# Kernel tuning notes

Measured on AMD Instinct MI355X. Metric: run time of the kernel, lower is better.

Reference implementation:

```python
import jax, jax.numpy as jnp
import numpy as np

EPS = 1e-8

def cos_sim(a, b, axis=-1):
    # torch.nn.functional.cosine_similarity: dot / max(|a|*|b|, eps)
    num = jnp.sum(a * b, axis=axis)
    den = jnp.maximum(jnp.linalg.norm(a, axis=axis) * jnp.linalg.norm(b, axis=axis), EPS)
    return num / den

def address_similarity(address, addresses):
    # address: [b, d], addresses: [b, n, d] -> [b, n]
    return cos_sim(address[:, None, :], addresses, axis=2)

def kv_insert(state_k, state_v, k, x, eps=EPS):
    # state_k/state_v: [b, n, d]; k: [b, d]; x: [b, d] (or [1, d], broadcast)
    alpha = cos_sim(k[:, None, :], state_k, axis=2)          # [b, n]
    alpha = jnp.where(alpha > eps, alpha, 0.0)
    return (1.0 - alpha)[..., None] * state_v + alpha[..., None] * x[:, None, :]

def replace(new_value, prev_value, tensr):
    # new_value/prev_value: [b, d]; tensr: [b, n, d]
    sim_to = cos_sim(prev_value[:, None, :], tensr, axis=2)  # [b, n]
    return tensr * (1.0 - sim_to)[..., None] + sim_to[..., None] * new_value[:, None, :]

def select_address(address, addresses, list_of_values):
    cs = address_similarity(address, addresses)              # [b, n]
    return [jnp.sum(values * cs[..., None], axis=1) for values in list_of_values]

def setup_inputs() -> dict:
    key = jax.random.key(0)
    ks = jax.random.split(key, 5)
    B, N, D = 32, 2048, 128
    return {
        "at_addr": jax.random.normal(ks[0], (B, D), dtype=jnp.float32),
        "addresses": jax.random.normal(ks[1], (B, N, D), dtype=jnp.float32),
        "tags": jax.random.normal(ks[2], (B, N, D), dtype=jnp.float32),
        "col1": jax.random.normal(ks[3], (B, N, D), dtype=jnp.float32),
        "col2": jax.random.normal(ks[4], (B, N, D), dtype=jnp.float32),
        "zero_vec": jnp.zeros((D,), dtype=jnp.float32),
        "gc_steps": 2,
    }

def reference(at_addr, addresses, tags, col1, col2, zero_vec, gc_steps):
    B = at_addr.shape[0]
    zv = jnp.broadcast_to(zero_vec[None, :], (B, zero_vec.shape[0]))
    # dereference the App node
    fn_addr, arg_addr = select_address(at_addr, addresses, [col1, col2])
    fn_tag, param_addr, body_addr = select_address(fn_addr, addresses, [tags, col1, col2])
    a_tag, a_l, a_r = select_address(arg_addr, addresses, [tags, col1, col2])
    # substitute arg into param's slot (globally scoped vars)
    tags = kv_insert(addresses, tags, param_addr, a_tag)
    col1 = kv_insert(addresses, col1, param_addr, a_l)
    col2 = kv_insert(addresses, col2, param_addr, a_r)
    col1 = replace(arg_addr, param_addr, col1)
    col2 = replace(arg_addr, param_addr, col2)
    # write the fn body over the App node
    b_tag, b_l, b_r = select_address(body_addr, addresses, [tags, col1, col2])
    tags = kv_insert(addresses, tags, at_addr, b_tag)
    col1 = kv_insert(addresses, col1, at_addr, b_l)
    col2 = kv_insert(addresses, col2, at_addr, b_r)
    # garbage collection
    for _ in range(gc_steps):
        for gaddr in (fn_addr, param_addr, body_addr):
            tags = kv_insert(addresses, tags, gaddr, zv)
            col1 = kv_insert(addresses, col1, gaddr, zv)
            col2 = kv_insert(addresses, col2, gaddr, zv)
    return (tags, col1, col2)
```

## Files before the change

### kernel.cpp

```cpp
#include <hip/hip_runtime.h>

#define EPSF 1e-8f
#define DD 128

__device__ __forceinline__ float4 ld4(const float* p){ return *reinterpret_cast<const float4*>(p); }
__device__ __forceinline__ void st4(float* p, const float4& v){ *reinterpret_cast<float4*>(p) = v; }
__device__ __forceinline__ float dot4(const float4& a, const float4& b){
  return a.x*b.x + a.y*b.y + a.z*b.z + a.w*b.w;
}
__device__ __forceinline__ void fma4(float4& acc, const float4& a, float s){
  acc.x += a.x*s; acc.y += a.y*s; acc.z += a.z*s; acc.w += a.w*s;
}
__device__ __forceinline__ float4 mix4(float a, const float4& v, const float4& x){
  float4 r;
  r.x = (1.f-a)*v.x + a*x.x;
  r.y = (1.f-a)*v.y + a*x.y;
  r.z = (1.f-a)*v.z + a*x.z;
  r.w = (1.f-a)*v.w + a*x.w;
  return r;
}
__device__ __forceinline__ float red16(float v){
  v += __shfl_xor(v, 1);
  v += __shfl_xor(v, 2);
  v += __shfl_xor(v, 4);
  v += __shfl_xor(v, 8);
  return v;
}
__device__ __forceinline__ void block_red16(float* red, int g, int l, int t,
                                            const float4& accA, const float4& accB,
                                            float* dst){
  red[g*DD + l*4+0] = accA.x;
  red[g*DD + l*4+1] = accA.y;
  red[g*DD + l*4+2] = accA.z;
  red[g*DD + l*4+3] = accA.w;
  red[g*DD + 64 + l*4+0] = accB.x;
  red[g*DD + 64 + l*4+1] = accB.y;
  red[g*DD + 64 + l*4+2] = accB.z;
  red[g*DD + 64 + l*4+3] = accB.w;
  __syncthreads();
  if (t < DD){
    float s = 0.f;
    #pragma unroll
    for (int q = 0; q < 16; ++q) s += red[q*DD + t];
    dst[t] = s;
  }
  __syncthreads();
}

__global__ __launch_bounds__(256) void kA(const float* __restrict__ at,
                                          const float* __restrict__ addr,
                                          const float* __restrict__ col1,
                                          const float* __restrict__ col2,
                                          float* __restrict__ cs0,
                                          float* __restrict__ naf,
                                          float* __restrict__ part,
                                          int B, int N, int chunks){
  __shared__ float red[16*DD];
  int blk = blockIdx.x;
  int b = blk / chunks, c = blk % chunks;
  int rows = N / chunks, n0 = c * rows;
  int t = threadIdx.x, g = t >> 4, l = t & 15;
  size_t bN = (size_t)b * N;

  const float* atp = at + (size_t)b*DD;
  float4 atA = ld4(atp + l*4), atB = ld4(atp + 64 + l*4);
  float nat = sqrtf(red16(dot4(atA, atA) + dot4(atB, atB)));

  float4 accFA = make_float4(0,0,0,0), accFB = accFA, accAA = accFA, accAB = accFA;
  #pragma unroll 2
  for (int r = g; r < rows; r += 16){
    size_t n = (size_t)n0 + r;
    size_t base = (bN + n)*DD;
    float4 aA  = ld4(addr + base + l*4), aB  = ld4(addr + base + 64 + l*4);
    float4 c1A = ld4(col1 + base + l*4), c1B = ld4(col1 + base + 64 + l*4);
    float4 c2A = ld4(col2 + base + l*4), c2B = ld4(col2 + base + 64 + l*4);
    float dp = red16(dot4(atA, aA) + dot4(atB, aB));
    float n2 = red16(dot4(aA, aA) + dot4(aB, aB));
    float na = sqrtf(n2);
    float cs = dp / fmaxf(nat * na, EPSF);
    if (l == 0){ cs0[bN + n] = cs; naf[bN + n] = na; }
    fma4(accFA, c1A, cs); fma4(accFB, c1B, cs);
    fma4(accAA, c2A, cs); fma4(accAB, c2B, cs);
  }
  block_red16(red, g, l, t, accFA, accFB, part + (((size_t)(0*B + b))*chunks + c)*DD);
  block_red16(red, g, l, t, accAA, accAB, part + (((size_t)(1*B + b))*chunks + c)*DD);
}

__global__ void kFin(const float* __restrict__ part, float* __restrict__ dst,
                     int nvec, int B, int chunks){
  int i = blockIdx.x*blockDim.x + threadIdx.x;
  int total = nvec * B * DD;
  if (i >= total) return;
  int d = i & (DD-1);
  int vb = i >> 7;
  const float* p = part + ((size_t)vb*chunks)*DD + d;
  float s = 0.f;
  for (int c = 0; c < chunks; ++c) s += p[(size_t)c*DD];
  dst[i] = s;
}

__global__ __launch_bounds__(256) void kB(const float* __restrict__ addr,
                                          const float* __restrict__ tags,
                                          const float* __restrict__ col1,
                                          const float* __restrict__ col2,
                                          const float* __restrict__ vecs,
                                          const float* __restrict__ naf,
                                          float* __restrict__ csfn,
                                          float* __restrict__ part,
                                          int B, int N, int chunks){
  __shared__ float red[16*DD];
  int blk = blockIdx.x;
  int b = blk / chunks, c = blk % chunks;
  int rows = N / chunks, n0 = c * rows;
  int t = threadIdx.x, g = t >> 4, l = t & 15;
  size_t bN = (size_t)b * N;

  const float* fnp = vecs + ((size_t)0*B + b)*DD;
  const float* agp = vecs + ((size_t)1*B + b)*DD;
  float4 fnA = ld4(fnp + l*4), fnB = ld4(fnp + 64 + l*4);
  float4 agA = ld4(agp + l*4), agB = ld4(agp + 64 + l*4);
  float nfn = sqrtf(red16(dot4(fnA, fnA) + dot4(fnB, fnB)));
  float nag = sqrtf(red16(dot4(agA, agA) + dot4(agB, agB)));

  float4 z = make_float4(0,0,0,0);
  float4 accPA=z, accPB=z, accBA=z, accBB=z, accTA=z, accTB=z, accLA=z, accLB=z, accRA=z, accRB=z;
  #pragma unroll 2
  for (int r = g; r < rows; r += 16){
    size_t n = (size_t)n0 + r;
    size_t base = (bN + n)*DD;
    float4 aA  = ld4(addr + base + l*4), aB  = ld4(addr + base + 64 + l*4);
    float4 t4A = ld4(tags + base + l*4), t4B = ld4(tags + base + 64 + l*4);
    float4 c1A = ld4(col1 + base + l*4), c1B = ld4(col1 + base + 64 + l*4);
    float4 c2A = ld4(col2 + base + l*4), c2B = ld4(col2 + base + 64 + l*4);
    float na = naf[bN + n];
    float dfn = red16(dot4(fnA, aA) + dot4(fnB, aB));
    float dag = red16(dot4(agA, aA) + dot4(agB, aB));
    float cf = dfn / fmaxf(nfn*na, EPSF);
    float ca = dag / fmaxf(nag*na, EPSF);
    if (l == 0) csfn[bN + n] = cf;
    fma4(accPA, c1A, cf); fma4(accPB, c1B, cf);
    fma4(accBA, c2A, cf); fma4(accBB, c2B, cf);
    fma4(accTA, t4A, ca); fma4(accTB, t4B, ca);
    fma4(accLA, c1A, ca); fma4(accLB, c1B, ca);
    fma4(accRA, c2A, ca); fma4(accRB, c2B, ca);
  }
  block_red16(red, g, l, t, accPA, accPB, part + (((size_t)(0*B + b))*chunks + c)*DD);
  block_red16(red, g, l, t, accBA, accBB, part + (((size_t)(1*B + b))*chunks + c)*DD);
  block_red16(red, g, l, t, accTA, accTB, part + (((size_t)(2*B + b))*chunks + c)*DD);
  block_red16(red, g, l, t, accLA, accLB, part + (((size_t)(3*B + b))*chunks + c)*DD);
  block_red16(red, g, l, t, accRA, accRB, part + (((size_t)(4*B + b))*chunks + c)*DD);
}

__global__ __launch_bounds__(256) void kC(const float* __restrict__ addr,
                                          const float* __restrict__ tags,
                                          const float* __restrict__ col1,
                                          const float* __restrict__ col2,
                                          const float* __restrict__ vecs,
                                          const float* __restrict__ naf,
                                          float* __restrict__ alphap,
                                          float* __restrict__ csbody,
                                          float* __restrict__ s1f,
                                          float* __restrict__ s2f,
                                          float* __restrict__ part,
                                          int B, int N, int chunks){
  __shared__ float red[16*DD];
  int blk = blockIdx.x;
  int b = blk / chunks, c = blk % chunks;
  int rows = N / chunks, n0 = c * rows;
  int t = threadIdx.x, g = t >> 4, l = t & 15;
  size_t bN = (size_t)b * N;

  size_t BD = (size_t)B*DD;
  const float* vp = vecs + (size_t)b*DD;
  float4 agA = ld4(vp + 1*BD + l*4), agB = ld4(vp + 1*BD + 64 + l*4);
  float4 pmA = ld4(vp + 2*BD + l*4), pmB = ld4(vp + 2*BD + 64 + l*4);
  float4 bdA = ld4(vp + 3*BD + l*4), bdB = ld4(vp + 3*BD + 64 + l*4);
  float4 xtA = ld4(vp + 4*BD + l*4), xtB = ld4(vp + 4*BD + 64 + l*4);
  float4 xlA = ld4(vp + 5*BD + l*4), xlB = ld4(vp + 5*BD + 64 + l*4);
  float4 xrA = ld4(vp + 6*BD + l*4), xrB = ld4(vp + 6*BD + 64 + l*4);
  float npm = sqrtf(red16(dot4(pmA, pmA) + dot4(pmB, pmB)));
  float nbd = sqrtf(red16(dot4(bdA, bdA) + dot4(bdB, bdB)));

  float4 z = make_float4(0,0,0,0);
  float4 accTA=z, accTB=z, accLA=z, accLB=z, accRA=z, accRB=z;
  #pragma unroll 2
  for (int r = g; r < rows; r += 16){
    size_t n = (size_t)n0 + r;
    size_t base = (bN + n)*DD;
    float4 aA  = ld4(addr + base + l*4), aB  = ld4(addr + base + 64 + l*4);
    float4 t4A = ld4(tags + base + l*4), t4B = ld4(tags + base + 64 + l*4);
    float4 c1A = ld4(col1 + base + l*4), c1B = ld4(col1 + base + 64 + l*4);
    float4 c2A = ld4(col2 + base + l*4), c2B = ld4(col2 + base + 64 + l*4);
    float na = naf[bN + n];
    float dp = red16(dot4(pmA, aA) + dot4(pmB, aB));
    float db = red16(dot4(bdA, aA) + dot4(bdB, aB));
    float csp = dp / fmaxf(npm*na, EPSF);
    float ap  = csp > EPSF ? csp : 0.f;
    float csb = db / fmaxf(nbd*na, EPSF);

    float4 tnA  = mix4(ap, t4A, xtA), tnB  = mix4(ap, t4B, xtB);
    float4 c1nA = mix4(ap, c1A, xlA), c1nB = mix4(ap, c1B, xlB);
    float4 c2nA = mix4(ap, c2A, xrA), c2nB = mix4(ap, c2B, xrB);
    float d1  = red16(dot4(pmA, c1nA) + dot4(pmB, c1nB));
    float n21 = red16(dot4(c1nA, c1nA) + dot4(c1nB, c1nB));
    float s1 = d1 / fmaxf(npm * sqrtf(n21), EPSF);
    float4 c1fA = mix4(s1, c1nA, agA), c1fB = mix4(s1, c1nB, agB);
    float d2  = red16(dot4(pmA, c2nA) + dot4(pmB, c2nB));
    float n22 = red16(dot4(c2nA, c2nA) + dot4(c2nB, c2nB));
    float s2 = d2 / fmaxf(npm * sqrtf(n22), EPSF);
    float4 c2fA = mix4(s2, c2nA, agA), c2fB = mix4(s2, c2nB, agB);

    if (l == 0){
      alphap[bN + n] = ap;
      csbody[bN + n] = csb;
      s1f[bN + n] = s1;
      s2f[bN + n] = s2;
    }
    fma4(accTA, tnA,  csb); fma4(accTB, tnB,  csb);
    fma4(accLA, c1fA, csb); fma4(accLB, c1fB, csb);
    fma4(accRA, c2fA, csb); fma4(accRB, c2fB, csb);
  }
  block_red16(red, g, l, t, accTA, accTB, part + (((size_t)(0*B + b))*chunks + c)*DD);
  block_red16(red, g, l, t, accLA, accLB, part + (((size_t)(1*B + b))*chunks + c)*DD);
  block_red16(red, g, l, t, accRA, accRB, part + (((size_t)(2*B + b))*chunks + c)*DD);
}

__global__ __launch_bounds__(256) void kE(const float* __restrict__ tags,
                                          const float* __restrict__ col1,
                                          const float* __restrict__ col2,
                                          float* __restrict__ o_t,
                                          float* __restrict__ o_1,
                                          float* __restrict__ o_2,
                                          const float* __restrict__ cs0,
                                          const float* __restrict__ csfn,
                                          const float* __restrict__ alphap,
                                          const float* __restrict__ csbody,
                                          const float* __restrict__ s1f,
                                          const float* __restrict__ s2f,
                                          const float* __restrict__ vecs,
                                          const float* __restrict__ zv,
                                          const int* __restrict__ gcp,
                                          int B, int N){
  size_t i = (size_t)blockIdx.x*blockDim.x + threadIdx.x;
  size_t total = (size_t)B*N*(DD/4);
  if (i >= total) return;
  int l = (int)(i & 31);
  size_t bn = i >> 5;
  int b = (int)(bn / (size_t)N);

  float ap = alphap[bn], s1 = s1f[bn], s2 = s2f[bn];
  float c0 = cs0[bn], cf = csfn[bn], cb = csbody[bn];
  float aat = c0 > EPSF ? c0 : 0.f;
  float af  = cf > EPSF ? cf : 0.f;
  float ab  = cb > EPSF ? cb : 0.f;
  float q = (1.f-af)*(1.f-ap)*(1.f-ab);
  int gc = gcp[0];
  float P = 1.f;
  for (int k = 0; k < gc; ++k) P *= q;

  size_t BD = (size_t)B*DD;
  const float* vb = vecs + (size_t)b*DD + (size_t)l*4;
  float4 ag = ld4(vb + 1*BD);
  float4 xt = ld4(vb + 4*BD), xl = ld4(vb + 5*BD), xr = ld4(vb + 6*BD);
  float4 bt = ld4(vb + 7*BD), bl = ld4(vb + 8*BD), br = ld4(vb + 9*BD);
  float4 z4 = ld4(zv + l*4);

  size_t off = bn*DD + (size_t)l*4;
  float4 t4 = ld4(tags + off), c1 = ld4(col1 + off), c2 = ld4(col2 + off);

  float4 tn  = mix4(ap, t4, xt);
  float4 c1f = mix4(s1, mix4(ap, c1, xl), ag);
  float4 c2f = mix4(s2, mix4(ap, c2, xr), ag);

  float4 u;
  u = mix4(aat, tn, bt);
  u.x = P*u.x + (1.f-P)*z4.x; u.y = P*u.y + (1.f-P)*z4.y;
  u.z = P*u.z + (1.f-P)*z4.z; u.w = P*u.w + (1.f-P)*z4.w;
  st4(o_t + off, u);
  u = mix4(aat, c1f, bl);
  u.x = P*u.x + (1.f-P)*z4.x; u.y = P*u.y + (1.f-P)*z4.y;
  u.z = P*u.z + (1.f-P)*z4.z; u.w = P*u.w + (1.f-P)*z4.w;
  st4(o_1 + off, u);
  u = mix4(aat, c2f, br);
  u.x = P*u.x + (1.f-P)*z4.x; u.y = P*u.y + (1.f-P)*z4.y;
  u.z = P*u.z + (1.f-P)*z4.z; u.w = P*u.w + (1.f-P)*z4.w;
  st4(o_2 + off, u);
}

extern "C" void kernel_launch(void* const* d_in, const int* in_sizes, int n_in,
                              void* d_out, int out_size, void* d_ws, size_t ws_size,
                              hipStream_t stream){
  const float* at   = (const float*)d_in[0];
  const float* addr = (const float*)d_in[1];
  const float* tags = (const float*)d_in[2];
  const float* col1 = (const float*)d_in[3];
  const float* col2 = (const float*)d_in[4];
  const float* zv   = (const float*)d_in[5];
  const int*   gc   = (const int*)d_in[6];

  int Dd = in_sizes[5];
  int B  = in_sizes[0] / Dd;
  int N  = in_sizes[1] / in_sizes[0];
  (void)Dd;

  size_t S  = (size_t)B * N;
  size_t BD = (size_t)B * DD;

  int CH = 32;
  while (CH > 1){
    size_t need = (7*S + 10*BD + (size_t)5*B*CH*DD) * sizeof(float);
    if (need <= ws_size && (N % CH) == 0) break;
    CH >>= 1;
  }

  float* w = (float*)d_ws;
  float* cs0    = w;
  float* csfn   = w + S;
  float* alphap = w + 2*S;
  float* csbody = w + 3*S;
  float* s1f    = w + 4*S;
  float* s2f    = w + 5*S;
  float* naf    = w + 6*S;
  float* vecs   = w + 7*S;
  float* part   = vecs + 10*BD;

  float* o_t = (float*)d_out;
  float* o_1 = o_t + (size_t)B*N*DD;
  float* o_2 = o_1 + (size_t)B*N*DD;

  dim3 blk(256);
  dim3 grid(B*CH);

  kA<<<grid, blk, 0, stream>>>(at, addr, col1, col2, cs0, naf, part, B, N, CH);
  {
    int tot = 2*B*DD;
    kFin<<<(tot+255)/256, 256, 0, stream>>>(part, vecs + 0*BD, 2, B, CH);
  }
  kB<<<grid, blk, 0, stream>>>(addr, tags, col1, col2, vecs, naf, csfn, part, B, N, CH);
  {
    int tot = 5*B*DD;
    kFin<<<(tot+255)/256, 256, 0, stream>>>(part, vecs + 2*BD, 5, B, CH);
  }
  kC<<<grid, blk, 0, stream>>>(addr, tags, col1, col2, vecs, naf, alphap, csbody,
                               s1f, s2f, part, B, N, CH);
  {
    int tot = 3*B*DD;
    kFin<<<(tot+255)/256, 256, 0, stream>>>(part, vecs + 7*BD, 3, B, CH);
  }
  {
    size_t tot = (size_t)B*N*(DD/4);
    kE<<<(unsigned)((tot+255)/256), 256, 0, stream>>>(tags, col1, col2, o_t, o_1, o_2,
                                                      cs0, csfn, alphap, csbody,
                                                      s1f, s2f, vecs, zv, gc, B, N);
  }
}
```

Before: 126.3 us.

## Fuse all phases into one cooperative persistent kernel with grid syncs

Replaces the separate similarity, partial-reduce and final-update kernels with one cooperative kernel. The phases are separated by grid.sync(), so launch gaps between the seven stages go away. The final update is remapped so each block writes the same row chunk it processed earlier, which may improve cache reuse. In exchange it adds six grid-wide barriers and caps the grid size by occupancy, with a register limit from launch_bounds(256,4); a per-phase multi-launch fallback remains if the cooperative launch fails.

Measured after the change: 450.0 us. +256.5%, slower.

```diff
diff --git a/kernel.cpp b/kernel.cpp
--- a/kernel.cpp
+++ b/kernel.cpp
@@ -1,4 +1,7 @@
 #include <hip/hip_runtime.h>
+#include <hip/hip_cooperative_groups.h>
+
+namespace cg = cooperative_groups;
 
 #define EPSF 1e-8f
 #define DD 128
@@ -47,244 +50,230 @@
   __syncthreads();
 }
 
-__global__ __launch_bounds__(256) void kA(const float* __restrict__ at,
-                                          const float* __restrict__ addr,
-                                          const float* __restrict__ col1,
-                                          const float* __restrict__ col2,
-                                          float* __restrict__ cs0,
-                                          float* __restrict__ naf,
-                                          float* __restrict__ part,
-                                          int B, int N, int chunks){
+__global__ __launch_bounds__(256, 4) void kFused(
+    const float* __restrict__ at,   const float* __restrict__ addr,
+    const float* __restrict__ tags, const float* __restrict__ col1,
+    const float* __restrict__ col2, const float* __restrict__ zv,
+    const int* __restrict__ gcp,
+    float* __restrict__ o_t, float* __restrict__ o_1, float* __restrict__ o_2,
+    float* __restrict__ w, int B, int N, int CH, int onlyPhase)
+{
+  cg::grid_group grid = cg::this_grid();
   __shared__ float red[16*DD];
-  int blk = blockIdx.x;
-  int b = blk / chunks, c = blk % chunks;
-  int rows = N / chunks, n0 = c * rows;
-  int t = threadIdx.x, g = t >> 4, l = t & 15;
-  size_t bN = (size_t)b * N;
-
-  const float* atp = at + (size_t)b*DD;
-  float4 atA = ld4(atp + l*4), atB = ld4(atp + 64 + l*4);
-  float nat = sqrtf(red16(dot4(atA, atA) + dot4(atB, atB)));
-
-  float4 accFA = make_float4(0,0,0,0), accFB = accFA, accAA = accFA, accAB = accFA;
-  #pragma unroll 2
-  for (int r = g; r < rows; r += 16){
-    size_t n = (size_t)n0 + r;
-    size_t base = (bN + n)*DD;
-    float4 aA  = ld4(addr + base + l*4), aB  = ld4(addr + base + 64 + l*4);
-    float4 c1A = ld4(col1 + base + l*4), c1B = ld4(col1 + base + 64 + l*4);
-    float4 c2A = ld4(col2 + base + l*4), c2B = ld4(col2 + base + 64 + l*4);
-    float dp = red16(dot4(atA, aA) + dot4(atB, aB));
-    float n2 = red16(dot4(aA, aA) + dot4(aB, aB));
-    float na = sqrtf(n2);
-    float cs = dp / fmaxf(nat * na, EPSF);
-    if (l == 0){ cs0[bN + n] = cs; naf[bN + n] = na; }
-    fma4(accFA, c1A, cs); fma4(accFB, c1B, cs);
-    fma4(accAA, c2A, cs); fma4(accAB, c2B, cs);
-  }
-  block_red16(red, g, l, t, accFA, accFB, part + (((size_t)(0*B + b))*chunks + c)*DD);
-  block_red16(red, g, l, t, accAA, accAB, part + (((size_t)(1*B + b))*chunks + c)*DD);
-}
-
-__global__ void kFin(const float* __restrict__ part, float* __restrict__ dst,
-                     int nvec, int B, int chunks){
-  int i = blockIdx.x*blockDim.x + threadIdx.x;
-  int total = nvec * B * DD;
-  if (i >= total) return;
-  int d = i & (DD-1);
-  int vb = i >> 7;
-  const float* p = part + ((size_t)vb*chunks)*DD + d;
-  float s = 0.f;
-  for (int c = 0; c < chunks; ++c) s += p[(size_t)c*DD];
-  dst[i] = s;
-}
-
-__global__ __launch_bounds__(256) void kB(const float* __restrict__ addr,
-                                          const float* __restrict__ tags,
-                                          const float* __restrict__ col1,
-                                          const float* __restrict__ col2,
-                                          const float* __restrict__ vecs,
-                                          const float* __restrict__ naf,
-                                          float* __restrict__ csfn,
-                                          float* __restrict__ part,
-                                          int B, int N, int chunks){
-  __shared__ float red[16*DD];
-  int blk = blockIdx.x;
-  int b = blk / chunks, c = blk % chunks;
-  int rows = N / chunks, n0 = c * rows;
-  int t = threadIdx.x, g = t >> 4, l = t & 15;
-  size_t bN = (size_t)b * N;
-
-  const float* fnp = vecs + ((size_t)0*B + b)*DD;
-  const float* agp = vecs + ((size_t)1*B + b)*DD;
-  float4 fnA = ld4(fnp + l*4), fnB = ld4(fnp + 64 + l*4);
-  float4 agA = ld4(agp + l*4), agB = ld4(agp + 64 + l*4);
-  float nfn = sqrtf(red16(dot4(fnA, fnA) + dot4(fnB, fnB)));
-  float nag = sqrtf(red16(dot4(agA, agA) + dot4(agB, agB)));
-
-  float4 z = make_float4(0,0,0,0);
-  float4 accPA=z, accPB=z, accBA=z, accBB=z, accTA=z, accTB=z, accLA=z, accLB=z, accRA=z, accRB=z;
-  #pragma unroll 2
-  for (int r = g; r < rows; r += 16){
-    size_t n = (size_t)n0 + r;
-    size_t base = (bN + n)*DD;
-    float4 aA  = ld4(addr + base + l*4), aB  = ld4(addr + base + 64 + l*4);
-    float4 t4A = ld4(tags + base + l*4), t4B = ld4(tags + base + 64 + l*4);
-    float4 c1A = ld4(col1 + base + l*4), c1B = ld4(col1 + base + 64 + l*4);
-    float4 c2A = ld4(col2 + base + l*4), c2B = ld4(col2 + base + 64 + l*4);
-    float na = naf[bN + n];
-    float dfn = red16(dot4(fnA, aA) + dot4(fnB, aB));
-    float dag = red16(dot4(agA, aA) + dot4(agB, aB));
-    float cf = dfn / fmaxf(nfn*na, EPSF);
-    float ca = dag / fmaxf(nag*na, EPSF);
-    if (l == 0) csfn[bN + n] = cf;
-    fma4(accPA, c1A, cf); fma4(accPB, c1B, cf);
-    fma4(accBA, c2A, cf); fma4(accBB, c2B, cf);
-    fma4(accTA, t4A, ca); fma4(accTB, t4B, ca);
-    fma4(accLA, c1A, ca); fma4(accLB, c1B, ca);
-    fma4(accRA, c2A, ca); fma4(accRB, c2B, ca);
-  }
-  block_red16(red, g, l, t, accPA, accPB, part + (((size_t)(0*B + b))*chunks + c)*DD);
-  block_red16(red, g, l, t, accBA, accBB, part + (((size_t)(1*B + b))*chunks + c)*DD);
-  block_red16(red, g, l, t, accTA, accTB, part + (((size_t)(2*B + b))*chunks + c)*DD);
-  block_red16(red, g, l, t, accLA, accLB, part + (((size_t)(3*B + b))*chunks + c)*DD);
-  block_red16(red, g, l, t, accRA, accRB, part + (((size_t)(4*B + b))*chunks + c)*DD);
-}
-
-__global__ __launch_bounds__(256) void kC(const float* __restrict__ addr,
-                                          const float* __restrict__ tags,
-                                          const float* __restrict__ col1,
-                                          const float* __restrict__ col2,
-                                          const float* __restrict__ vecs,
-                                          const float* __restrict__ naf,
-                                          float* __restrict__ alphap,
-                                          float* __restrict__ csbody,
-                                          float* __restrict__ s1f,
-                                          float* __restrict__ s2f,
-                                          float* __restrict__ part,
-                                          int B, int N, int chunks){
-  __shared__ float red[16*DD];
-  int blk = blockIdx.x;
-  int b = blk / chunks, c = blk % chunks;
-  int rows = N / chunks, n0 = c * rows;
-  int t = threadIdx.x, g = t >> 4, l = t & 15;
-  size_t bN = (size_t)b * N;
-
-  size_t BD = (size_t)B*DD;
-  const float* vp = vecs + (size_t)b*DD;
-  float4 agA = ld4(vp + 1*BD + l*4), agB = ld4(vp + 1*BD + 64 + l*4);
-  float4 pmA = ld4(vp + 2*BD + l*4), pmB = ld4(vp + 2*BD + 64 + l*4);
-  float4 bdA = ld4(vp + 3*BD + l*4), bdB = ld4(vp + 3*BD + 64 + l*4);
-  float4 xtA = ld4(vp + 4*BD + l*4), xtB = ld4(vp + 4*BD + 64 + l*4);
-  float4 xlA = ld4(vp + 5*BD + l*4), xlB = ld4(vp + 5*BD + 64 + l*4);
-  float4 xrA = ld4(vp + 6*BD + l*4), xrB = ld4(vp + 6*BD + 64 + l*4);
-  float npm = sqrtf(red16(dot4(pmA, pmA) + dot4(pmB, pmB)));
-  float nbd = sqrtf(red16(dot4(bdA, bdA) + dot4(bdB, bdB)));
-
-  float4 z = make_float4(0,0,0,0);
-  float4 accTA=z, accTB=z, accLA=z, accLB=z, accRA=z, accRB=z;
-  #pragma unroll 2
-  for (int r = g; r < rows; r += 16){
-    size_t n = (size_t)n0 + r;
-    size_t base = (bN + n)*DD;
-    float4 aA  = ld4(addr + base + l*4), aB  = ld4(addr + base + 64 + l*4);
-    float4 t4A = ld4(tags + base + l*4), t4B = ld4(tags + base + 64 + l*4);
-    float4 c1A = ld4(col1 + base + l*4), c1B = ld4(col1 + base + 64 + l*4);
-    float4 c2A = ld4(col2 + base + l*4), c2B = ld4(col2 + base + 64 + l*4);
-    float na = naf[bN + n];
-    float dp = red16(dot4(pmA, aA) + dot4(pmB, aB));
-    float db = red16(dot4(bdA, aA) + dot4(bdB, aB));
-    float csp = dp / fmaxf(npm*na, EPSF);
-    float ap  = csp > EPSF ? csp : 0.f;
-    float csb = db / fmaxf(nbd*na, EPSF);
-
-    float4 tnA  = mix4(ap, t4A, xtA), tnB  = mix4(ap, t4B, xtB);
-    float4 c1nA = mix4(ap, c1A, xlA), c1nB = mix4(ap, c1B, xlB);
-    float4 c2nA = mix4(ap, c2A, xrA), c2nB = mix4(ap, c2B, xrB);
-    float d1  = red16(dot4(pmA, c1nA) + dot4(pmB, c1nB));
-    float n21 = red16(dot4(c1nA, c1nA) + dot4(c1nB, c1nB));
-    float s1 = d1 / fmaxf(npm * sqrtf(n21), EPSF);
-    float4 c1fA = mix4(s1, c1nA, agA), c1fB = mix4(s1, c1nB, agB);
-    float d2  = red16(dot4(pmA, c2nA) + dot4(pmB, c2nB));
-    float n22 = red16(dot4(c2nA, c2nA) + dot4(c2nB, c2nB));
-    float s2 = d2 / fmaxf(npm * sqrtf(n22), EPSF);
-    float4 c2fA = mix4(s2, c2nA, agA), c2fB = mix4(s2, c2nB, agB);
-
-    if (l == 0){
-      alphap[bN + n] = ap;
-      csbody[bN + n] = csb;
-      s1f[bN + n] = s1;
-      s2f[bN + n] = s2;
-    }
-    fma4(accTA, tnA,  csb); fma4(accTB, tnB,  csb);
-    fma4(accLA, c1fA, csb); fma4(accLB, c1fB, csb);
-    fma4(accRA, c2fA, csb); fma4(accRB, c2fB, csb);
-  }
-  block_red16(red, g, l, t, accTA, accTB, part + (((size_t)(0*B + b))*chunks + c)*DD);
-  block_red16(red, g, l, t, accLA, accLB, part + (((size_t)(1*B + b))*chunks + c)*DD);
-  block_red16(red, g, l, t, accRA, accRB, part + (((size_t)(2*B + b))*chunks + c)*DD);
-}
-
-__global__ __launch_bounds__(256) void kE(const float* __restrict__ tags,
-                                          const float* __restrict__ col1,
-                                          const float* __restrict__ col2,
-                                          float* __restrict__ o_t,
-                                          float* __restrict__ o_1,
-                                          float* __restrict__ o_2,
-                                          const float* __restrict__ cs0,
-                                          const float* __restrict__ csfn,
-                                          const float* __restrict__ alphap,
-                                          const float* __restrict__ csbody,
-                                          const float* __restrict__ s1f,
-                                          const float* __restrict__ s2f,
-                                          const float* __restrict__ vecs,
-                                          const float* __restrict__ zv,
-                                          const int* __restrict__ gcp,
-                                          int B, int N){
-  size_t i = (size_t)blockIdx.x*blockDim.x + threadIdx.x;
-  size_t total = (size_t)B*N*(DD/4);
-  if (i >= total) return;
-  int l = (int)(i & 31);
-  size_t bn = i >> 5;
-  int b = (int)(bn / (size_t)N);
-
-  float ap = alphap[bn], s1 = s1f[bn], s2 = s2f[bn];
-  float c0 = cs0[bn], cf = csfn[bn], cb = csbody[bn];
-  float aat = c0 > EPSF ? c0 : 0.f;
-  float af  = cf > EPSF ? cf : 0.f;
-  float ab  = cb > EPSF ? cb : 0.f;
-  float q = (1.f-af)*(1.f-ap)*(1.f-ab);
-  int gc = gcp[0];
-  float P = 1.f;
-  for (int k = 0; k < gc; ++k) P *= q;
-
-  size_t BD = (size_t)B*DD;
-  const float* vb = vecs + (size_t)b*DD + (size_t)l*4;
-  float4 ag = ld4(vb + 1*BD);
-  float4 xt = ld4(vb + 4*BD), xl = ld4(vb + 5*BD), xr = ld4(vb + 6*BD);
-  float4 bt = ld4(vb + 7*BD), bl = ld4(vb + 8*BD), br = ld4(vb + 9*BD);
-  float4 z4 = ld4(zv + l*4);
-
-  size_t off = bn*DD + (size_t)l*4;
-  float4 t4 = ld4(tags + off), c1 = ld4(col1 + off), c2 = ld4(col2 + off);
-
-  float4 tn  = mix4(ap, t4, xt);
-  float4 c1f = mix4(s1, mix4(ap, c1, xl), ag);
-  float4 c2f = mix4(s2, mix4(ap, c2, xr), ag);
-
-  float4 u;
-  u = mix4(aat, tn, bt);
-  u.x = P*u.x + (1.f-P)*z4.x; u.y = P*u.y + (1.f-P)*z4.y;
-  u.z = P*u.z + (1.f-P)*z4.z; u.w = P*u.w + (1.f-P)*z4.w;
-  st4(o_t + off, u);
-  u = mix4(aat, c1f, bl);
-  u.x = P*u.x + (1.f-P)*z4.x; u.y = P*u.y + (1.f-P)*z4.y;
-  u.z = P*u.z + (1.f-P)*z4.z; u.w = P*u.w + (1.f-P)*z4.w;
-  st4(o_1 + off, u);
-  u = mix4(aat, c2f, br);
-  u.x = P*u.x + (1.f-P)*z4.x; u.y = P*u.y + (1.f-P)*z4.y;
-  u.z = P*u.z + (1.f-P)*z4.z; u.w = P*u.w + (1.f-P)*z4.w;
-  st4(o_2 + off, u);
+
+  const size_t S  = (size_t)B * N;
+  const size_t BD = (size_t)B * DD;
+  float* cs0    = w;
+  float* csfn   = w + S;
+  float* alphap = w + 2*S;
+  float* csbody = w + 3*S;
+  float* s1f    = w + 4*S;
+  float* s2f    = w + 5*S;
+  float* naf    = w + 6*S;
+  float* vecs   = w + 7*S;
+  float* part   = vecs + 10*BD;
+
+  const int blk = blockIdx.x;
+  const int b = blk / CH, c = blk % CH;
+  const int rows = N / CH, n0 = c * rows;
+  const int t = threadIdx.x, g = t >> 4, l = t & 15;
+  const size_t bN = (size_t)b * N;
+  const int G = gridDim.x;
+
+  if (onlyPhase < 0 || onlyPhase == 0){
+    const float* atp = at + (size_t)b*DD;
+    float4 atA = ld4(atp + l*4), atB = ld4(atp + 64 + l*4);
+    float nat = sqrtf(red16(dot4(atA, atA) + dot4(atB, atB)));
+    float4 accFA = make_float4(0,0,0,0), accFB = accFA, accAA = accFA, accAB = accFA;
+    #pragma unroll 2
+    for (int r = g; r < rows; r += 16){
+      size_t n = (size_t)n0 + r;
+      size_t base = (bN + n)*DD;
+      float4 aA  = ld4(addr + base + l*4), aB  = ld4(addr + base + 64 + l*4);
+      float4 c1A = ld4(col1 + base + l*4), c1B = ld4(col1 + base + 64 + l*4);
+      float4 c2A = ld4(col2 + base + l*4), c2B = ld4(col2 + base + 64 + l*4);
+      float dp = red16(dot4(atA, aA) + dot4(atB, aB));
+      float n2 = red16(dot4(aA, aA) + dot4(aB, aB));
+      float na = sqrtf(n2);
+      float cs = dp / fmaxf(nat * na, EPSF);
+      if (l == 0){ cs0[bN + n] = cs; naf[bN + n] = na; }
+      fma4(accFA, c1A, cs); fma4(accFB, c1B, cs);
+      fma4(accAA, c2A, cs); fma4(accAB, c2B, cs);
+    }
+    block_red16(red, g, l, t, accFA, accFB, part + ((size_t)(0*B + b)*CH + c)*DD);
+    block_red16(red, g, l, t, accAA, accAB, part + ((size_t)(1*B + b)*CH + c)*DD);
+  }
+  if (onlyPhase < 0) grid.sync();
+
+  if (onlyPhase < 0 || onlyPhase == 1){
+    int tot = 2*B*DD;
+    for (int i = blk*256 + t; i < tot; i += G*256){
+      int vb = i >> 7, d = i & (DD-1);
+      const float* p = part + ((size_t)vb*CH)*DD + d;
+      float s = 0.f;
+      for (int cc = 0; cc < CH; ++cc) s += p[(size_t)cc*DD];
+      vecs[i] = s;
+    }
+  }
+  if (onlyPhase < 0) grid.sync();
+
+  if (onlyPhase < 0 || onlyPhase == 2){
+    const float* fnp = vecs + (size_t)b*DD;
+    const float* agp = vecs + BD + (size_t)b*DD;
+    float4 fnA = ld4(fnp + l*4), fnB = ld4(fnp + 64 + l*4);
+    float4 agA = ld4(agp + l*4), agB = ld4(agp + 64 + l*4);
+    float nfn = sqrtf(red16(dot4(fnA, fnA) + dot4(fnB, fnB)));
+    float nag = sqrtf(red16(dot4(agA, agA) + dot4(agB, agB)));
+    float4 z = make_float4(0,0,0,0);
+    float4 accPA=z, accPB=z, accBA=z, accBB=z, accTA=z, accTB=z, accLA=z, accLB=z, accRA=z, accRB=z;
+    #pragma unroll 2
+    for (int r = g; r < rows; r += 16){
+      size_t n = (size_t)n0 + r;
+      size_t base = (bN + n)*DD;
+      float4 aA  = ld4(addr + base + l*4), aB  = ld4(addr + base + 64 + l*4);
+      float4 t4A = ld4(tags + base + l*4), t4B = ld4(tags + base + 64 + l*4);
+      float4 c1A = ld4(col1 + base + l*4), c1B = ld4(col1 + base + 64 + l*4);
+      float4 c2A = ld4(col2 + base + l*4), c2B = ld4(col2 + base + 64 + l*4);
+      float na = naf[bN + n];
+      float dfn = red16(dot4(fnA, aA) + dot4(fnB, aB));
+      float dag = red16(dot4(agA, aA) + dot4(agB, aB));
+      float cf = dfn / fmaxf(nfn*na, EPSF);
+      float ca = dag / fmaxf(nag*na, EPSF);
+      if (l == 0) csfn[bN + n] = cf;
+      fma4(accPA, c1A, cf); fma4(accPB, c1B, cf);
+      fma4(accBA, c2A, cf); fma4(accBB, c2B, cf);
+      fma4(accTA, t4A, ca); fma4(accTB, t4B, ca);
+      fma4(accLA, c1A, ca); fma4(accLB, c1B, ca);
+      fma4(accRA, c2A, ca); fma4(accRB, c2B, ca);
+    }
+    block_red16(red, g, l, t, accPA, accPB, part + ((size_t)(0*B + b)*CH + c)*DD);
+    block_red16(red, g, l, t, accBA, accBB, part + ((size_t)(1*B + b)*CH + c)*DD);
+    block_red16(red, g, l, t, accTA, accTB, part + ((size_t)(2*B + b)*CH + c)*DD);
+    block_red16(red, g, l, t, accLA, accLB, part + ((size_t)(3*B + b)*CH + c)*DD);
+    block_red16(red, g, l, t, accRA, accRB, part + ((size_t)(4*B + b)*CH + c)*DD);
+  }
+  if (onlyPhase < 0) grid.sync();
+
+  if (onlyPhase < 0 || onlyPhase == 3){
+    int tot = 5*B*DD;
+    for (int i = blk*256 + t; i < tot; i += G*256){
+      int vb = i >> 7, d = i & (DD-1);
+      const float* p = part + ((size_t)vb*CH)*DD + d;
+      float s = 0.f;
+      for (int cc = 0; cc < CH; ++cc) s += p[(size_t)cc*DD];
+      vecs[2*BD + i] = s;
+    }
+  }
+  if (onlyPhase < 0) grid.sync();
+
+  if (onlyPhase < 0 || onlyPhase == 4){
+    const float* vp = vecs + (size_t)b*DD;
+    float4 agA = ld4(vp + 1*BD + l*4), agB = ld4(vp + 1*BD + 64 + l*4);
+    float4 pmA = ld4(vp + 2*BD + l*4), pmB = ld4(vp + 2*BD + 64 + l*4);
+    float4 bdA = ld4(vp + 3*BD + l*4), bdB = ld4(vp + 3*BD + 64 + l*4);
+    float4 xtA = ld4(vp + 4*BD + l*4), xtB = ld4(vp + 4*BD + 64 + l*4);
+    float4 xlA = ld4(vp + 5*BD + l*4), xlB = ld4(vp + 5*BD + 64 + l*4);
+    float4 xrA = ld4(vp + 6*BD + l*4), xrB = ld4(vp + 6*BD + 64 + l*4);
+    float npm = sqrtf(red16(dot4(pmA, pmA) + dot4(pmB, pmB)));
+    float nbd = sqrtf(red16(dot4(bdA, bdA) + dot4(bdB, bdB)));
+    float4 z = make_float4(0,0,0,0);
+    float4 accTA=z, accTB=z, accLA=z, accLB=z, accRA=z, accRB=z;
+    #pragma unroll 2
+    for (int r = g; r < rows; r += 16){
+      size_t n = (size_t)n0 + r;
+      size_t base = (bN + n)*DD;
+      float4 aA  = ld4(addr + base + l*4), aB  = ld4(addr + base + 64 + l*4);
+      float4 t4A = ld4(tags + base + l*4), t4B = ld4(tags + base + 64 + l*4);
+      float4 c1A = ld4(col1 + base + l*4), c1B = ld4(col1 + base + 64 + l*4);
+      float4 c2A = ld4(col2 + base + l*4), c2B = ld4(col2 + base + 64 + l*4);
+      float na = naf[bN + n];
+      float dp = red16(dot4(pmA, aA) + dot4(pmB, aB));
+      float db = red16(dot4(bdA, aA) + dot4(bdB, aB));
+      float csp = dp / fmaxf(npm*na, EPSF);
+      float ap  = csp > EPSF ? csp : 0.f;
+      float csb = db / fmaxf(nbd*na, EPSF);
+
+      float4 tnA  = mix4(ap, t4A, xtA), tnB  = mix4(ap, t4B, xtB);
+      float4 c1nA = mix4(ap, c1A, xlA), c1nB = mix4(ap, c1B, xlB);
+      float4 c2nA = mix4(ap, c2A, xrA), c2nB = mix4(ap, c2B, xrB);
+      float d1  = red16(dot4(pmA, c1nA) + dot4(pmB, c1nB));
+      float n21 = red16(dot4(c1nA, c1nA) + dot4(c1nB, c1nB));
+      float s1 = d1 / fmaxf(npm * sqrtf(n21), EPSF);
+      float4 c1fA = mix4(s1, c1nA, agA), c1fB = mix4(s1, c1nB, agB);
+      float d2  = red16(dot4(pmA, c2nA) + dot4(pmB, c2nB));
+      float n22 = red16(dot4(c2nA, c2nA) + dot4(c2nB, c2nB));
+      float s2 = d2 / fmaxf(npm * sqrtf(n22), EPSF);
+      float4 c2fA = mix4(s2, c2nA, agA), c2fB = mix4(s2, c2nB, agB);
+
+      if (l == 0){
+        alphap[bN + n] = ap;
+        csbody[bN + n] = csb;
+        s1f[bN + n] = s1;
+        s2f[bN + n] = s2;
+      }
+      fma4(accTA, tnA,  csb); fma4(accTB, tnB,  csb);
+      fma4(accLA, c1fA, csb); fma4(accLB, c1fB, csb);
+      fma4(accRA, c2fA, csb); fma4(accRB, c2fB, csb);
+    }
+    block_red16(red, g, l, t, accTA, accTB, part + ((size_t)(0*B + b)*CH + c)*DD);
+    block_red16(red, g, l, t, accLA, accLB, part + ((size_t)(1*B + b)*CH + c)*DD);
+    block_red16(red, g, l, t, accRA, accRB, part + ((size_t)(2*B + b)*CH + c)*DD);
+  }
+  if (onlyPhase < 0) grid.sync();
+
+  if (onlyPhase < 0 || onlyPhase == 5){
+    int tot = 3*B*DD;
+    for (int i = blk*256 + t; i < tot; i += G*256){
+      int vb = i >> 7, d = i & (DD-1);
+      const float* p = part + ((size_t)vb*CH)*DD + d;
+      float s = 0.f;
+      for (int cc = 0; cc < CH; ++cc) s += p[(size_t)cc*DD];
+      vecs[7*BD + i] = s;
+    }
+  }
+  if (onlyPhase < 0) grid.sync();
+
+  if (onlyPhase < 0 || onlyPhase == 6){
+    const int l2 = t & 31;
+    const int r0 = t >> 5;
+    const float* vb = vecs + (size_t)b*DD + (size_t)l2*4;
+    float4 ag = ld4(vb + 1*BD);
+    float4 xt = ld4(vb + 4*BD), xl = ld4(vb + 5*BD), xr = ld4(vb + 6*BD);
+    float4 bt = ld4(vb + 7*BD), bl = ld4(vb + 8*BD), br = ld4(vb + 9*BD);
+    float4 z4 = ld4(zv + l2*4);
+    int gcn = gcp[0];
+    for (int r = r0; r < rows; r += 8){
+      size_t bn = bN + (size_t)n0 + r;
+      float ap = alphap[bn], s1 = s1f[bn], s2 = s2f[bn];
+      float c0 = cs0[bn], cf = csfn[bn], cb = csbody[bn];
+      float aat = c0 > EPSF ? c0 : 0.f;
+      float af  = cf > EPSF ? cf : 0.f;
+      float ab  = cb > EPSF ? cb : 0.f;
+      float q = (1.f-af)*(1.f-ap)*(1.f-ab);
+      float P = 1.f;
+      for (int k = 0; k < gcn; ++k) P *= q;
+
+      size_t off = bn*DD + (size_t)l2*4;
+      float4 t4 = ld4(tags + off), c1 = ld4(col1 + off), c2 = ld4(col2 + off);
+      float4 tn  = mix4(ap, t4, xt);
+      float4 c1f = mix4(s1, mix4(ap, c1, xl), ag);
+      float4 c2f = mix4(s2, mix4(ap, c2, xr), ag);
+
+      float4 u;
+      u = mix4(aat, tn, bt);
+      u.x = P*u.x + (1.f-P)*z4.x; u.y = P*u.y + (1.f-P)*z4.y;
+      u.z = P*u.z + (1.f-P)*z4.z; u.w = P*u.w + (1.f-P)*z4.w;
+      st4(o_t + off, u);
+      u = mix4(aat, c1f, bl);
+      u.x = P*u.x + (1.f-P)*z4.x; u.y = P*u.y + (1.f-P)*z4.y;
+      u.z = P*u.z + (1.f-P)*z4.z; u.w = P*u.w + (1.f-P)*z4.w;
+      st4(o_1 + off, u);
+      u = mix4(aat, c2f, br);
+      u.x = P*u.x + (1.f-P)*z4.x; u.y = P*u.y + (1.f-P)*z4.y;
+      u.z = P*u.z + (1.f-P)*z4.z; u.w = P*u.w + (1.f-P)*z4.w;
+      st4(o_2 + off, u);
+    }
+  }
 }
 
 extern "C" void kernel_launch(void* const* d_in, const int* in_sizes, int n_in,
@@ -306,51 +295,36 @@
   size_t S  = (size_t)B * N;
   size_t BD = (size_t)B * DD;
 
+  int maxB = 0;
+  if (hipOccupancyMaxActiveBlocksPerMultiprocessor(&maxB, kFused, 256, 0) != hipSuccess || maxB < 1)
+    maxB = 1;
+  long cap = (long)maxB * 256;
+
   int CH = 32;
   while (CH > 1){
-    size_t need = (7*S + 10*BD + (size_t)5*B*CH*DD) * sizeof(float);
-    if (need <= ws_size && (N % CH) == 0) break;
+    bool fitw = (7*S + 10*BD + (size_t)5*B*CH*DD) * sizeof(float) <= ws_size;
+    bool fitc = (long)B*CH <= cap;
+    if (fitw && fitc && (N % CH) == 0) break;
     CH >>= 1;
   }
-
-  float* w = (float*)d_ws;
-  float* cs0    = w;
-  float* csfn   = w + S;
-  float* alphap = w + 2*S;
-  float* csbody = w + 3*S;
-  float* s1f    = w + 4*S;
-  float* s2f    = w + 5*S;
-  float* naf    = w + 6*S;
-  float* vecs   = w + 7*S;
-  float* part   = vecs + 10*BD;
-
+  int G = B * CH;
+
+  float* w   = (float*)d_ws;
   float* o_t = (float*)d_out;
   float* o_1 = o_t + (size_t)B*N*DD;
   float* o_2 = o_1 + (size_t)B*N*DD;
 
-  dim3 blk(256);
-  dim3 grid(B*CH);
-
-  kA<<<grid, blk, 0, stream>>>(at, addr, col1, col2, cs0, naf, part, B, N, CH);
-  {
-    int tot = 2*B*DD;
-    kFin<<<(tot+255)/256, 256, 0, stream>>>(part, vecs + 0*BD, 2, B, CH);
-  }
-  kB<<<grid, blk, 0, stream>>>(addr, tags, col1, col2, vecs, naf, csfn, part, B, N, CH);
-  {
-    int tot = 5*B*DD;
-    kFin<<<(tot+255)/256, 256, 0, stream>>>(part, vecs + 2*BD, 5, B, CH);
-  }
-  kC<<<grid, blk, 0, stream>>>(addr, tags, col1, col2, vecs, naf, alphap, csbody,
-                               s1f, s2f, part, B, N, CH);
-  {
-    int tot = 3*B*DD;
-    kFin<<<(tot+255)/256, 256, 0, stream>>>(part, vecs + 7*BD, 3, B, CH);
-  }
-  {
-    size_t tot = (size_t)B*N*(DD/4);
-    kE<<<(unsigned)((tot+255)/256), 256, 0, stream>>>(tags, col1, col2, o_t, o_1, o_2,
-                                                      cs0, csfn, alphap, csbody,
-                                                      s1f, s2f, vecs, zv, gc, B, N);
-  }
-}
+  int onlyPhase = -1;
+  void* args[] = {(void*)&at, (void*)&addr, (void*)&tags, (void*)&col1, (void*)&col2,
+                  (void*)&zv, (void*)&gc, (void*)&o_t, (void*)&o_1, (void*)&o_2,
+                  (void*)&w, (void*)&B, (void*)&N, (void*)&CH, (void*)&onlyPhase};
+  hipError_t err = hipLaunchCooperativeKernel((const void*)kFused, dim3(G), dim3(256),
+                                              args, 0, stream);
+  if (err != hipSuccess){
+    for (int p = 0; p < 7; ++p){
+      hipLaunchKernelGGL(kFused, dim3(G), dim3(256), 0, stream,
+                         at, addr, tags, col1, col2, zv, gc,
+                         o_t, o_1, o_2, w, B, N, CH, p);
+    }
+  }
+}
```

## Fold partial-sum finalize kernels into consumer kernels via per-block reductions

Applied to the files above, without the earlier changes.

Removes the three kFin launches and instead has each consumer kernel (kB, kC, kE) reduce the per-chunk partial vectors it needs into shared memory at block start. Partial buffers are kept separate (partA/B/C) so later kernels can re-reduce earlier stages' results. kE is restructured into a per-(batch, chunk) grid that loops over rows, so the reduced vectors are loaded once per block. This saves launch and dependency gaps but makes every block redundantly re-reduce CH partials, which adds extra global reads.

Measured after the change: 204.3 us. 1.62x slower.

```diff
diff --git a/kernel.cpp b/kernel.cpp
--- a/kernel.cpp
+++ b/kernel.cpp
@@ -47,18 +47,30 @@
   __syncthreads();
 }
 
+__device__ __forceinline__ void reduce_vecs(const float* __restrict__ part, int B, int b,
+                                            int CH, int nv, float* vsm, int t){
+  for (int i = t; i < nv*DD; i += 256){
+    int v = i >> 7, d = i & (DD-1);
+    const float* p = part + ((size_t)(v*B + b)*CH)*DD + d;
+    float s = 0.f;
+    for (int c = 0; c < CH; ++c) s += p[(size_t)c*DD];
+    vsm[i] = s;
+  }
+  __syncthreads();
+}
+
 __global__ __launch_bounds__(256) void kA(const float* __restrict__ at,
                                           const float* __restrict__ addr,
                                           const float* __restrict__ col1,
                                           const float* __restrict__ col2,
                                           float* __restrict__ cs0,
                                           float* __restrict__ naf,
-                                          float* __restrict__ part,
-                                          int B, int N, int chunks){
+                                          float* __restrict__ partA,
+                                          int B, int N, int CH){
   __shared__ float red[16*DD];
   int blk = blockIdx.x;
-  int b = blk / chunks, c = blk % chunks;
-  int rows = N / chunks, n0 = c * rows;
+  int b = blk / CH, c = blk % CH;
+  int rows = N / CH, n0 = c * rows;
   int t = threadIdx.x, g = t >> 4, l = t & 15;
   size_t bN = (size_t)b * N;
 
@@ -82,43 +94,31 @@
     fma4(accFA, c1A, cs); fma4(accFB, c1B, cs);
     fma4(accAA, c2A, cs); fma4(accAB, c2B, cs);
   }
-  block_red16(red, g, l, t, accFA, accFB, part + (((size_t)(0*B + b))*chunks + c)*DD);
-  block_red16(red, g, l, t, accAA, accAB, part + (((size_t)(1*B + b))*chunks + c)*DD);
-}
-
-__global__ void kFin(const float* __restrict__ part, float* __restrict__ dst,
-                     int nvec, int B, int chunks){
-  int i = blockIdx.x*blockDim.x + threadIdx.x;
-  int total = nvec * B * DD;
-  if (i >= total) return;
-  int d = i & (DD-1);
-  int vb = i >> 7;
-  const float* p = part + ((size_t)vb*chunks)*DD + d;
-  float s = 0.f;
-  for (int c = 0; c < chunks; ++c) s += p[(size_t)c*DD];
-  dst[i] = s;
+  block_red16(red, g, l, t, accFA, accFB, partA + ((size_t)(0*B + b)*CH + c)*DD);
+  block_red16(red, g, l, t, accAA, accAB, partA + ((size_t)(1*B + b)*CH + c)*DD);
 }
 
 __global__ __launch_bounds__(256) void kB(const float* __restrict__ addr,
                                           const float* __restrict__ tags,
                                           const float* __restrict__ col1,
                                           const float* __restrict__ col2,
-                                          const float* __restrict__ vecs,
+                                          const float* __restrict__ partA,
                                           const float* __restrict__ naf,
                                           float* __restrict__ csfn,
-                                          float* __restrict__ part,
-                                          int B, int N, int chunks){
+                                          float* __restrict__ partB,
+                                          int B, int N, int CH){
   __shared__ float red[16*DD];
+  __shared__ float vsm[2*DD];
   int blk = blockIdx.x;
-  int b = blk / chunks, c = blk % chunks;
-  int rows = N / chunks, n0 = c * rows;
+  int b = blk / CH, c = blk % CH;
+  int rows = N / CH, n0 = c * rows;
   int t = threadIdx.x, g = t >> 4, l = t & 15;
   size_t bN = (size_t)b * N;
 
-  const float* fnp = vecs + ((size_t)0*B + b)*DD;
-  const float* agp = vecs + ((size_t)1*B + b)*DD;
-  float4 fnA = ld4(fnp + l*4), fnB = ld4(fnp + 64 + l*4);
-  float4 agA = ld4(agp + l*4), agB = ld4(agp + 64 + l*4);
+  reduce_vecs(partA, B, b, CH, 2, vsm, t);
+
+  float4 fnA = ld4(vsm + l*4),      fnB = ld4(vsm + 64 + l*4);
+  float4 agA = ld4(vsm + DD + l*4), agB = ld4(vsm + DD + 64 + l*4);
   float nfn = sqrtf(red16(dot4(fnA, fnA) + dot4(fnB, fnB)));
   float nag = sqrtf(red16(dot4(agA, agA) + dot4(agB, agB)));
 
@@ -144,40 +144,43 @@
     fma4(accLA, c1A, ca); fma4(accLB, c1B, ca);
     fma4(accRA, c2A, ca); fma4(accRB, c2B, ca);
   }
-  block_red16(red, g, l, t, accPA, accPB, part + (((size_t)(0*B + b))*chunks + c)*DD);
-  block_red16(red, g, l, t, accBA, accBB, part + (((size_t)(1*B + b))*chunks + c)*DD);
-  block_red16(red, g, l, t, accTA, accTB, part + (((size_t)(2*B + b))*chunks + c)*DD);
-  block_red16(red, g, l, t, accLA, accLB, part + (((size_t)(3*B + b))*chunks + c)*DD);
-  block_red16(red, g, l, t, accRA, accRB, part + (((size_t)(4*B + b))*chunks + c)*DD);
+  block_red16(red, g, l, t, accPA, accPB, partB + ((size_t)(0*B + b)*CH + c)*DD);
+  block_red16(red, g, l, t, accBA, accBB, partB + ((size_t)(1*B + b)*CH + c)*DD);
+  block_red16(red, g, l, t, accTA, accTB, partB + ((size_t)(2*B + b)*CH + c)*DD);
+  block_red16(red, g, l, t, accLA, accLB, partB + ((size_t)(3*B + b)*CH + c)*DD);
+  block_red16(red, g, l, t, accRA, accRB, partB + ((size_t)(4*B + b)*CH + c)*DD);
 }
 
 __global__ __launch_bounds__(256) void kC(const float* __restrict__ addr,
                                           const float* __restrict__ tags,
                                           const float* __restrict__ col1,
                                           const float* __restrict__ col2,
-                                          const float* __restrict__ vecs,
+                                          const float* __restrict__ partA,
+                                          const float* __restrict__ partB,
                                           const float* __restrict__ naf,
                                           float* __restrict__ alphap,
                                           float* __restrict__ csbody,
                                           float* __restrict__ s1f,
                                           float* __restrict__ s2f,
-                                          float* __restrict__ part,
-                                          int B, int N, int chunks){
+                                          float* __restrict__ partC,
+                                          int B, int N, int CH){
   __shared__ float red[16*DD];
+  __shared__ float vsm[6*DD];
   int blk = blockIdx.x;
-  int b = blk / chunks, c = blk % chunks;
-  int rows = N / chunks, n0 = c * rows;
+  int b = blk / CH, c = blk % CH;
+  int rows = N / CH, n0 = c * rows;
   int t = threadIdx.x, g = t >> 4, l = t & 15;
   size_t bN = (size_t)b * N;
 
-  size_t BD = (size_t)B*DD;
-  const float* vp = vecs + (size_t)b*DD;
-  float4 agA = ld4(vp + 1*BD + l*4), agB = ld4(vp + 1*BD + 64 + l*4);
-  float4 pmA = ld4(vp + 2*BD + l*4), pmB = ld4(vp + 2*BD + 64 + l*4);
-  float4 bdA = ld4(vp + 3*BD + l*4), bdB = ld4(vp + 3*BD + 64 + l*4);
-  float4 xtA = ld4(vp + 4*BD + l*4), xtB = ld4(vp + 4*BD + 64 + l*4);
-  float4 xlA = ld4(vp + 5*BD + l*4), xlB = ld4(vp + 5*BD + 64 + l*4);
-  float4 xrA = ld4(vp + 6*BD + l*4), xrB = ld4(vp + 6*BD + 64 + l*4);
+  reduce_vecs(partA + (size_t)(1*B)*CH*DD, B, b, CH, 1, vsm, t);
+  reduce_vecs(partB, B, b, CH, 5, vsm + DD, t);
+
+  float4 agA = ld4(vsm + 0*DD + l*4), agB = ld4(vsm + 0*DD + 64 + l*4);
+  float4 pmA = ld4(vsm + 1*DD + l*4), pmB = ld4(vsm + 1*DD + 64 + l*4);
+  float4 bdA = ld4(vsm + 2*DD + l*4), bdB = ld4(vsm + 2*DD + 64 + l*4);
+  float4 xtA = ld4(vsm + 3*DD + l*4), xtB = ld4(vsm + 3*DD + 64 + l*4);
+  float4 xlA = ld4(vsm + 4*DD + l*4), xlB = ld4(vsm + 4*DD + 64 + l*4);
+  float4 xrA = ld4(vsm + 5*DD + l*4), xrB = ld4(vsm + 5*DD + 64 + l*4);
   float npm = sqrtf(red16(dot4(pmA, pmA) + dot4(pmB, pmB)));
   float nbd = sqrtf(red16(dot4(bdA, bdA) + dot4(bdB, bdB)));
 
@@ -220,9 +223,9 @@
     fma4(accLA, c1fA, csb); fma4(accLB, c1fB, csb);
     fma4(accRA, c2fA, csb); fma4(accRB, c2fB, csb);
   }
-  block_red16(red, g, l, t, accTA, accTB, part + (((size_t)(0*B + b))*chunks + c)*DD);
-  block_red16(red, g, l, t, accLA, accLB, part + (((size_t)(1*B + b))*chunks + c)*DD);
-  block_red16(red, g, l, t, accRA, accRB, part + (((size_t)(2*B + b))*chunks + c)*DD);
+  block_red16(red, g, l, t, accTA, accTB, partC + ((size_t)(0*B + b)*CH + c)*DD);
+  block_red16(red, g, l, t, accLA, accLB, partC + ((size_t)(1*B + b)*CH + c)*DD);
+  block_red16(red, g, l, t, accRA, accRB, partC + ((size_t)(2*B + b)*CH + c)*DD);
 }
 
 __global__ __launch_bounds__(256) void kE(const float* __restrict__ tags,
@@ -237,54 +240,62 @@
                                           const float* __restrict__ csbody,
                                           const float* __restrict__ s1f,
                                           const float* __restrict__ s2f,
-                                          const float* __restrict__ vecs,
+                                          const float* __restrict__ partA,
+                                          const float* __restrict__ partB,
+                                          const float* __restrict__ partC,
                                           const float* __restrict__ zv,
                                           const int* __restrict__ gcp,
-                                          int B, int N){
-  size_t i = (size_t)blockIdx.x*blockDim.x + threadIdx.x;
-  size_t total = (size_t)B*N*(DD/4);
-  if (i >= total) return;
-  int l = (int)(i & 31);
-  size_t bn = i >> 5;
-  int b = (int)(bn / (size_t)N);
-
-  float ap = alphap[bn], s1 = s1f[bn], s2 = s2f[bn];
-  float c0 = cs0[bn], cf = csfn[bn], cb = csbody[bn];
-  float aat = c0 > EPSF ? c0 : 0.f;
-  float af  = cf > EPSF ? cf : 0.f;
-  float ab  = cb > EPSF ? cb : 0.f;
-  float q = (1.f-af)*(1.f-ap)*(1.f-ab);
-  int gc = gcp[0];
-  float P = 1.f;
-  for (int k = 0; k < gc; ++k) P *= q;
-
-  size_t BD = (size_t)B*DD;
-  const float* vb = vecs + (size_t)b*DD + (size_t)l*4;
-  float4 ag = ld4(vb + 1*BD);
-  float4 xt = ld4(vb + 4*BD), xl = ld4(vb + 5*BD), xr = ld4(vb + 6*BD);
-  float4 bt = ld4(vb + 7*BD), bl = ld4(vb + 8*BD), br = ld4(vb + 9*BD);
-  float4 z4 = ld4(zv + l*4);
-
-  size_t off = bn*DD + (size_t)l*4;
-  float4 t4 = ld4(tags + off), c1 = ld4(col1 + off), c2 = ld4(col2 + off);
-
-  float4 tn  = mix4(ap, t4, xt);
-  float4 c1f = mix4(s1, mix4(ap, c1, xl), ag);
-  float4 c2f = mix4(s2, mix4(ap, c2, xr), ag);
-
-  float4 u;
-  u = mix4(aat, tn, bt);
-  u.x = P*u.x + (1.f-P)*z4.x; u.y = P*u.y + (1.f-P)*z4.y;
-  u.z = P*u.z + (1.f-P)*z4.z; u.w = P*u.w + (1.f-P)*z4.w;
-  st4(o_t + off, u);
-  u = mix4(aat, c1f, bl);
-  u.x = P*u.x + (1.f-P)*z4.x; u.y = P*u.y + (1.f-P)*z4.y;
-  u.z = P*u.z + (1.f-P)*z4.z; u.w = P*u.w + (1.f-P)*z4.w;
-  st4(o_1 + off, u);
-  u = mix4(aat, c2f, br);
-  u.x = P*u.x + (1.f-P)*z4.x; u.y = P*u.y + (1.f-P)*z4.y;
-  u.z = P*u.z + (1.f-P)*z4.z; u.w = P*u.w + (1.f-P)*z4.w;
-  st4(o_2 + off, u);
+                                          int B, int N, int CH){
+  __shared__ float vsm[7*DD];
+  int blk = blockIdx.x;
+  int b = blk / CH, c = blk % CH;
+  int rows = N / CH, n0 = c * rows;
+  int t = threadIdx.x;
+  size_t bN = (size_t)b * N;
+
+  reduce_vecs(partA + (size_t)(1*B)*CH*DD, B, b, CH, 1, vsm, t);
+  reduce_vecs(partB + (size_t)(2*B)*CH*DD, B, b, CH, 3, vsm + DD, t);
+  reduce_vecs(partC, B, b, CH, 3, vsm + 4*DD, t);
+
+  const int l2 = t & 31;
+  const int r0 = t >> 5;
+  float4 ag = ld4(vsm + 0*DD + l2*4);
+  float4 xt = ld4(vsm + 1*DD + l2*4), xl = ld4(vsm + 2*DD + l2*4), xr = ld4(vsm + 3*DD + l2*4);
+  float4 bt = ld4(vsm + 4*DD + l2*4), bl = ld4(vsm + 5*DD + l2*4), br = ld4(vsm + 6*DD + l2*4);
+  float4 z4 = ld4(zv + l2*4);
+  int gcn = gcp[0];
+
+  for (int r = r0; r < rows; r += 8){
+    size_t bn = bN + (size_t)n0 + r;
+    float ap = alphap[bn], s1 = s1f[bn], s2 = s2f[bn];
+    float c0 = cs0[bn], cf = csfn[bn], cb = csbody[bn];
+    float aat = c0 > EPSF ? c0 : 0.f;
+    float af  = cf > EPSF ? cf : 0.f;
+    float ab  = cb > EPSF ? cb : 0.f;
+    float q = (1.f-af)*(1.f-ap)*(1.f-ab);
+    float P = 1.f;
+    for (int k = 0; k < gcn; ++k) P *= q;
+
+    size_t off = bn*DD + (size_t)l2*4;
+    float4 t4 = ld4(tags + off), c1 = ld4(col1 + off), c2 = ld4(col2 + off);
+    float4 tn  = mix4(ap, t4, xt);
+    float4 c1f = mix4(s1, mix4(ap, c1, xl), ag);
+    float4 c2f = mix4(s2, mix4(ap, c2, xr), ag);
+
+    float4 u;
+    u = mix4(aat, tn, bt);
+    u.x = P*u.x + (1.f-P)*z4.x; u.y = P*u.y + (1.f-P)*z4.y;
+    u.z = P*u.z + (1.f-P)*z4.z; u.w = P*u.w + (1.f-P)*z4.w;
+    st4(o_t + off, u);
+    u = mix4(aat, c1f, bl);
+    u.x = P*u.x + (1.f-P)*z4.x; u.y = P*u.y + (1.f-P)*z4.y;
+    u.z = P*u.z + (1.f-P)*z4.z; u.w = P*u.w + (1.f-P)*z4.w;
+    st4(o_1 + off, u);
+    u = mix4(aat, c2f, br);
+    u.x = P*u.x + (1.f-P)*z4.x; u.y = P*u.y + (1.f-P)*z4.y;
+    u.z = P*u.z + (1.f-P)*z4.z; u.w = P*u.w + (1.f-P)*z4.w;
+    st4(o_2 + off, u);
+  }
 }
 
 extern "C" void kernel_launch(void* const* d_in, const int* in_sizes, int n_in,
@@ -304,11 +315,10 @@
   (void)Dd;
 
   size_t S  = (size_t)B * N;
-  size_t BD = (size_t)B * DD;
 
   int CH = 32;
   while (CH > 1){
-    size_t need = (7*S + 10*BD + (size_t)5*B*CH*DD) * sizeof(float);
+    size_t need = (7*S + (size_t)10*B*CH*DD) * sizeof(float);
     if (need <= ws_size && (N % CH) == 0) break;
     CH >>= 1;
   }
@@ -321,8 +331,9 @@
   float* s1f    = w + 4*S;
   float* s2f    = w + 5*S;
   float* naf    = w + 6*S;
-  float* vecs   = w + 7*S;
-  float* part   = vecs + 10*BD;
+  float* partA  = w + 7*S;
+  float* partB  = partA + (size_t)2*B*CH*DD;
+  float* partC  = partB + (size_t)5*B*CH*DD;
 
   float* o_t = (float*)d_out;
   float* o_1 = o_t + (size_t)B*N*DD;
@@ -331,26 +342,11 @@
   dim3 blk(256);
   dim3 grid(B*CH);
 
-  kA<<<grid, blk, 0, stream>>>(at, addr, col1, col2, cs0, naf, part, B, N, CH);
-  {
-    int tot = 2*B*DD;
-    kFin<<<(tot+255)/256, 256, 0, stream>>>(part, vecs + 0*BD, 2, B, CH);
-  }
-  kB<<<grid, blk, 0, stream>>>(addr, tags, col1, col2, vecs, naf, csfn, part, B, N, CH);
-  {
-    int tot = 5*B*DD;
-    kFin<<<(tot+255)/256, 256, 0, stream>>>(part, vecs + 2*BD, 5, B, CH);
-  }
-  kC<<<grid, blk, 0, stream>>>(addr, tags, col1, col2, vecs, naf, alphap, csbody,
-                               s1f, s2f, part, B, N, CH);
-  {
-    int tot = 3*B*DD;
-    kFin<<<(tot+255)/256, 256, 0, stream>>>(part, vecs + 7*BD, 3, B, CH);
-  }
-  {
-    size_t tot = (size_t)B*N*(DD/4);
-    kE<<<(unsigned)((tot+255)/256), 256, 0, stream>>>(tags, col1, col2, o_t, o_1, o_2,
-                                                      cs0, csfn, alphap, csbody,
-                                                      s1f, s2f, vecs, zv, gc, B, N);
-  }
-}
+  kA<<<grid, blk, 0, stream>>>(at, addr, col1, col2, cs0, naf, partA, B, N, CH);
+  kB<<<grid, blk, 0, stream>>>(addr, tags, col1, col2, partA, naf, csfn, partB, B, N, CH);
+  kC<<<grid, blk, 0, stream>>>(addr, tags, col1, col2, partA, partB, naf,
+                               alphap, csbody, s1f, s2f, partC, B, N, CH);
+  kE<<<grid, blk, 0, stream>>>(tags, col1, col2, o_t, o_1, o_2,
+                               cs0, csfn, alphap, csbody, s1f, s2f,
+                               partA, partB, partC, zv, gc, B, N, CH);
+}
```
